# Optimization experiments

Measured on AMD Instinct MI355X. Metric: run time of the kernel, lower is better.

## Reference

```python
import math
import jax, jax.numpy as jnp
import numpy as np

ANCHORS_SETTINGS = (
    dict(layer='p3', stride=32, size=48, scale=[2 ** (1.0 / 3.0), 2 ** (2.0 / 3.0)], aspect_ratio=[0.667, 1, 1.5]),
    dict(layer='p4', stride=64, size=96, scale=[2 ** (1.0 / 3.0), 2 ** (2.0 / 3.0)], aspect_ratio=[0.667, 1, 1.5]),
    dict(layer='p5', stride=128, size=192, scale=[1, 2 ** (1.0 / 3.0), 2 ** (2.0 / 3.0)], aspect_ratio=[0.667, 1, 1.5]),
)


def anchor_configs():
    # 21 static (kernel, stride, padding) configs, in the exact counter order of
    # weighted_anchor_aggregator (p3 x6, p4 x6, p5 x9).
    cfgs = []
    for info in ANCHORS_SETTINGS:
        stride, size = info['stride'], info['size']
        for scale in info['scale']:
            for ar in info['aspect_ratio']:
                kernel = (int(size * scale / float(ar) ** 0.5), int(size * scale * float(ar) ** 0.5))
                padding = (math.ceil((kernel[0] - stride) / 2.0), math.ceil((kernel[1] - stride) / 2.0))
                cfgs.append((kernel, (stride, stride), padding))
    return cfgs


def extract_weighted_patches(x, weights, kernel, stride, padding):
    # x: (B,H,W,C); weights: (B,k,gh,gw). Vectorized equivalent of the original
    # lax.scan over per-position dynamic_slice gathers:
    #   acc = sum_{i,j} weights[:,:,i,j] (x) x_pad[:, i*s : i*s+kh, j*s : j*s+kw, :]
    b = x.shape[0]
    _, k, gh, gw = weights.shape
    xp = jnp.pad(x, ((0, 0),
                     (padding[0], padding[0] + kernel[0]),
                     (padding[1], padding[1] + kernel[1]),
                     (0, 0)))
    rows = jnp.arange(gh)[:, None] * stride[0] + jnp.arange(kernel[0])[None, :]  # (gh, kh)
    cols = jnp.arange(gw)[:, None] * stride[1] + jnp.arange(kernel[1])[None, :]  # (gw, kw)
    # gather all strided patches: (B, gh, kh, gw, kw, C)
    patches = xp[:, rows][:, :, :, cols]
    # weighted sum over grid positions -> (B, k, kh, kw, C)
    return jnp.einsum('bkij,bihjwc->bkhwc', weights, patches)


def _aggregate(x, weights_p3, weights_p4, weights_p5):
    weights = ([weights_p3[:, a] for a in range(weights_p3.shape[1])]
               + [weights_p4[:, a] for a in range(weights_p4.shape[1])]
               + [weights_p5[:, a] for a in range(weights_p5.shape[1])])
    b, k = weights[0].shape[0], weights[0].shape[1]
    acc = jnp.zeros((b * k, 224, 224, 3), x.dtype)
    for w, (kernel, stride, padding) in zip(weights, anchor_configs()):
        agg = extract_weighted_patches(x, w, kernel, stride, padding)
        agg = agg.reshape(b * k, kernel[0], kernel[1], 3)
        acc = acc + jax.image.resize(agg, (b * k, 224, 224, 3), 'bilinear')
    return acc


def setup_inputs() -> dict:
    key = jax.random.key(0)
    k0, k1, k2, k3 = jax.random.split(key, 4)
    B, K = 8, 4
    return {
        'x': jax.random.normal(k0, (B, 448, 448, 3), jnp.float32),
        'weights_p3': jax.random.uniform(k1, (B, 6, K, 14, 14), jnp.float32),
        'weights_p4': jax.random.uniform(k2, (B, 6, K, 7, 7), jnp.float32),
        'weights_p5': jax.random.uniform(k3, (B, 9, K, 4, 4), jnp.float32),
    }


def reference(x, weights_p3, weights_p4, weights_p5):
    return _aggregate(x, weights_p3, weights_p4, weights_p5)
```

## Files before the change

kernel.cpp:

```cpp
#include <hip/hip_runtime.h>
#include <math.h>


#define BATCH 8
#define KK 4
#define OUT_HW 224
#define IMG_HW 448
#define NCFG 21

#define WTBL_BYTES (NCFG * 2 * OUT_HW * 16)
#define ITBL_BYTES (NCFG * 2 * OUT_HW * 4)
#define WT_OFF_BYTES (WTBL_BYTES + ITBL_BYTES)
#define WT_F4 12912
#define AGG_OFF_BYTES (WT_OFF_BYTES + WT_F4 * 16)

struct CfgEntry {
    int kh, kw;
    int mth, mtw;
    int tbl;
    int ws_off;
};

struct GroupArgs {
    CfgEntry e[NCFG];
    int n;
};

struct ACfg {
    int kh, kw, p0, p1;
    int layer;
    int qpr;
    int wt_off;
    int ws_off;
    int block_start;
    int blocks_per_img;
};

struct AggArgs {
    ACfg e[NCFG];
    int n;
};

struct TablesArgs { int kh[NCFG]; int kw[NCFG]; };

struct TrArgs {
    int layer[NCFG];
    int anchor[NCFG];
    int gsz[NCFG];
    int wt_off[NCFG];
};

struct F3 { float a, b, c; };

__device__ inline unsigned int bf16_rne(float f) {
    unsigned int u = __float_as_uint(f);
    return (u + 0x7fffu + ((u >> 16) & 1u)) >> 16;
}

__global__ __launch_bounds__(256) void init_tables(float4* __restrict__ wtbl,
                                                   int* __restrict__ itbl,
                                                   TablesArgs t) {
    int cfg = blockIdx.x >> 1;
    int dim = blockIdx.x & 1;
    int o = threadIdx.x;
    if (o >= OUT_HW) return;
    int n = dim ? t.kw[cfg] : t.kh[cfg];

    float inv = (float)(1.0 / ((double)OUT_HW / (double)n));
    float ks  = inv > 1.f ? inv : 1.f;
    float rks = 1.f / ks;
    float sf  = ((float)o + 0.5f) * inv - 0.5f;
    int i0 = (int)ceilf(sf - ks);  if (i0 < 0) i0 = 0;
    int i1 = (int)floorf(sf + ks); if (i1 > n - 1) i1 = n - 1;
    float sum = 0.f;
    for (int i = i0; i <= i1; ++i) {
        float v = 1.f - fabsf((float)i - sf) * rks;
        sum += (v > 0.f ? v : 0.f);
    }
    float rsum = 1.f / sum;
    float w[4];
#pragma unroll
    for (int d = 0; d < 4; ++d) {
        int i = i0 + d;
        float v = 0.f;
        if (i <= i1) {
            v = 1.f - fabsf((float)i - sf) * rks;
            v = (v > 0.f ? v : 0.f) * rsum;
        }
        w[d] = v;
    }
    int idx = cfg * (2 * OUT_HW) + dim * OUT_HW + o;
    wtbl[idx] = make_float4(w[0], w[1], w[2], w[3]);
    itbl[idx] = i0;
}

__global__ __launch_bounds__(256) void transpose_w(
        const float* __restrict__ wp3, const float* __restrict__ wp4,
        const float* __restrict__ wp5, float4* __restrict__ wT, TrArgs t) {
    int cfg = blockIdx.x;
    int b = blockIdx.y;
    int gsz = t.gsz[cfg];
    const float* base;
    int A;
    if (t.layer[cfg] == 0)      { base = wp3; A = 6; }
    else if (t.layer[cfg] == 1) { base = wp4; A = 6; }
    else                        { base = wp5; A = 9; }
    const float* src = base + (size_t)(b * A + t.anchor[cfg]) * (KK * gsz);
    for (int g = threadIdx.x; g < gsz; g += 256) {
        wT[t.wt_off[cfg] + b * gsz + g] =
            make_float4(src[0 * gsz + g], src[1 * gsz + g],
                        src[2 * gsz + g], src[3 * gsz + g]);
    }
}

template <int GH, int GW, int STRIDE>
__device__ inline void agg_body(const ACfg& c, int b, int h, int w0,
                                const float* __restrict__ xb,
                                const float4* __restrict__ wlds,
                                uint2* __restrict__ agg) {
    float acc[2][4][3] = {};

    const int rb = h - c.p0;
    int ilo = rb >= 0 ? 0 : (-rb + STRIDE - 1) / STRIDE;
    int ihi = (IMG_HW - 1 - rb) / STRIDE;
    if (ihi > GH - 1) ihi = GH - 1;

    const int cb = w0 - c.p1;

#pragma unroll 1
    for (int i = ilo; i <= ihi; ++i) {
        const float* xr = xb + (size_t)(rb + i * STRIDE) * (IMG_HW * 3);
        const float4* wrow = wlds + i * GW;
#pragma unroll
        for (int j = 0; j < GW; ++j) {
            int col = cb + j * STRIDE;
            int cc0 = col;
            if (cc0 < 0) cc0 = 0;
            if (cc0 > IMG_HW - 1) cc0 = IMG_HW - 1;
            int cc1 = col + 1;
            if (cc1 < 0) cc1 = 0;
            if (cc1 > IMG_HW - 1) cc1 = IMG_HW - 1;
            F3 v0 = *(const F3*)(xr + (size_t)cc0 * 3);
            F3 v1 = *(const F3*)(xr + (size_t)cc1 * 3);
            bool k0 = (unsigned)col < (unsigned)IMG_HW;
            bool k1 = (unsigned)(col + 1) < (unsigned)IMG_HW;
            float x0 = k0 ? v0.a : 0.f;
            float x1 = k0 ? v0.b : 0.f;
            float x2 = k0 ? v0.c : 0.f;
            float y0 = k1 ? v1.a : 0.f;
            float y1 = k1 ? v1.b : 0.f;
            float y2 = k1 ? v1.c : 0.f;
            float4 wk = wrow[j];
            acc[0][0][0] = fmaf(wk.x, x0, acc[0][0][0]);
            acc[0][0][1] = fmaf(wk.x, x1, acc[0][0][1]);
            acc[0][0][2] = fmaf(wk.x, x2, acc[0][0][2]);
            acc[0][1][0] = fmaf(wk.y, x0, acc[0][1][0]);
            acc[0][1][1] = fmaf(wk.y, x1, acc[0][1][1]);
            acc[0][1][2] = fmaf(wk.y, x2, acc[0][1][2]);
            acc[0][2][0] = fmaf(wk.z, x0, acc[0][2][0]);
            acc[0][2][1] = fmaf(wk.z, x1, acc[0][2][1]);
            acc[0][2][2] = fmaf(wk.z, x2, acc[0][2][2]);
            acc[0][3][0] = fmaf(wk.w, x0, acc[0][3][0]);
            acc[0][3][1] = fmaf(wk.w, x1, acc[0][3][1]);
            acc[0][3][2] = fmaf(wk.w, x2, acc[0][3][2]);
            acc[1][0][0] = fmaf(wk.x, y0, acc[1][0][0]);
            acc[1][0][1] = fmaf(wk.x, y1, acc[1][0][1]);
            acc[1][0][2] = fmaf(wk.x, y2, acc[1][0][2]);
            acc[1][1][0] = fmaf(wk.y, y0, acc[1][1][0]);
            acc[1][1][1] = fmaf(wk.y, y1, acc[1][1][1]);
            acc[1][1][2] = fmaf(wk.y, y2, acc[1][1][2]);
            acc[1][2][0] = fmaf(wk.z, y0, acc[1][2][0]);
            acc[1][2][1] = fmaf(wk.z, y1, acc[1][2][1]);
            acc[1][2][2] = fmaf(wk.z, y2, acc[1][2][2]);
            acc[1][3][0] = fmaf(wk.w, y0, acc[1][3][0]);
            acc[1][3][1] = fmaf(wk.w, y1, acc[1][3][1]);
            acc[1][3][2] = fmaf(wk.w, y2, acc[1][3][2]);
        }
    }

    const int npix = c.kh * c.kw;
    const bool two = (w0 + 1) < c.kw;
#pragma unroll
    for (int k = 0; k < 4; ++k) {
        size_t base = (size_t)c.ws_off + (size_t)(b * KK + k) * npix
                    + (size_t)h * c.kw + w0;
        uint2 o0;
        o0.x = bf16_rne(acc[0][k][0]) | (bf16_rne(acc[0][k][1]) << 16);
        o0.y = bf16_rne(acc[0][k][2]);
        agg[base] = o0;
        if (two) {
            uint2 o1;
            o1.x = bf16_rne(acc[1][k][0]) | (bf16_rne(acc[1][k][1]) << 16);
            o1.y = bf16_rne(acc[1][k][2]);
            agg[base + 1] = o1;
        }
    }
}

__global__ __launch_bounds__(256, 4) void agg_all(
        const float* __restrict__ x,
        const float4* __restrict__ wT,
        uint2* __restrict__ agg,
        AggArgs a) {
    int bid = blockIdx.x;
    int ci = 0;
    while (ci + 1 < a.n && bid >= a.e[ci + 1].block_start) ci++;
    const ACfg c = a.e[ci];
    int local = bid - c.block_start;
    int b     = local / c.blocks_per_img;
    int sblk  = local - b * c.blocks_per_img;

    const int gsz = (c.layer == 0) ? 196 : (c.layer == 1) ? 49 : 16;
    __shared__ float4 wlds[196];
    for (int t = threadIdx.x; t < gsz; t += 256)
        wlds[t] = wT[c.wt_off + b * gsz + t];
    __syncthreads();

    int pidx = sblk * 256 + (int)threadIdx.x;
    if (pidx >= c.kh * c.qpr) return;
    int h  = pidx / c.qpr;
    int w0 = (pidx - h * c.qpr) * 2;

    const float* __restrict__ xb = x + (size_t)b * (IMG_HW * IMG_HW * 3);
    if (c.layer == 0)      agg_body<14, 14, 32>(c, b, h, w0, xb, wlds, agg);
    else if (c.layer == 1) agg_body<7, 7, 64>(c, b, h, w0, xb, wlds, agg);
    else                   agg_body<4, 4, 128>(c, b, h, w0, xb, wlds, agg);
}

template <int TH, int TW>
__device__ inline void taps_direct(const uint2* __restrict__ base,
                                   int kh, int kw, int i0, int j0,
                                   float4 wh4, float4 ww4,
                                   float& a0, float& a1, float& a2) {
    const float* wh = (const float*)&wh4;
    const float* ww = (const float*)&ww4;
    uint2 v[TH][TW];
#pragma unroll
    for (int d = 0; d < TH; ++d) {
        int gi = i0 + d;
        if (gi > kh - 1) gi = kh - 1;
        const uint2* rp = base + (size_t)gi * kw;
#pragma unroll
        for (int e = 0; e < TW; ++e) {
            int gj = j0 + e;
            if (gj > kw - 1) gj = kw - 1;
            v[d][e] = rp[gj];
        }
    }
#pragma unroll
    for (int d = 0; d < TH; ++d) {
        float r0 = 0.f, r1 = 0.f, r2 = 0.f;
#pragma unroll
        for (int e = 0; e < TW; ++e) {
            uint2 t = v[d][e];
            float c0 = __uint_as_float(t.x << 16);
            float c1 = __uint_as_float(t.x & 0xffff0000u);
            float c2 = __uint_as_float(t.y << 16);
            float w = ww[e];
            r0 = fmaf(w, c0, r0);
            r1 = fmaf(w, c1, r1);
            r2 = fmaf(w, c2, r2);
        }
        a0 = fmaf(wh[d], r0, a0);
        a1 = fmaf(wh[d], r1, a1);
        a2 = fmaf(wh[d], r2, a2);
    }
}

__global__ __launch_bounds__(256) void resize_kernel(
        const uint2* __restrict__ agg,
        const float4* __restrict__ wtbl,
        const int* __restrict__ itbl,
        float* __restrict__ out,
        GroupArgs g, int accumulate) {
    const int tid = threadIdx.x;
    const int tx = tid & 15;
    const int ty = tid >> 4;
    const int xo = blockIdx.x * 16 + tx;
    const int yo = blockIdx.y * 16 + ty;
    const int bk = blockIdx.z;

    __shared__ float4 wlds[NCFG * 32];
    __shared__ int    ilds[NCFG * 32];

    const int nent = g.n * 32;
    for (int e = tid; e < nent; e += 256) {
        int ci  = e >> 5;
        int r   = e & 31;
        int isW = r >> 4;
        int idx = r & 15;
        int base_o = isW ? (blockIdx.x * 16) : (blockIdx.y * 16);
        int src = g.e[ci].tbl * (2 * OUT_HW) + isW * OUT_HW + base_o + idx;
        wlds[ci * 32 + r] = wtbl[src];
        ilds[ci * 32 + r] = itbl[src];
    }
    __syncthreads();

    size_t ob = (((size_t)bk * OUT_HW + yo) * OUT_HW + xo) * 3;
    float a0, a1, a2;
    if (accumulate) {
        a0 = out[ob]; a1 = out[ob + 1]; a2 = out[ob + 2];
    } else {
        a0 = a1 = a2 = 0.f;
    }

    for (int c = 0; c < g.n; ++c) {
        const CfgEntry e = g.e[c];
        float4 wh4 = wlds[c * 32 + ty];
        float4 ww4 = wlds[c * 32 + 16 + tx];
        int i0 = ilds[c * 32 + ty];
        int j0 = ilds[c * 32 + 16 + tx];
        const uint2* base = agg + (size_t)e.ws_off
                          + (size_t)bk * ((size_t)e.kh * e.kw);

        switch ((e.mth << 2) | e.mtw) {
            case (2 << 2) | 2:
                taps_direct<2, 2>(base, e.kh, e.kw, i0, j0, wh4, ww4, a0, a1, a2);
                break;
            case (3 << 2) | 2:
                taps_direct<3, 2>(base, e.kh, e.kw, i0, j0, wh4, ww4, a0, a1, a2);
                break;
            case (2 << 2) | 3:
                taps_direct<2, 3>(base, e.kh, e.kw, i0, j0, wh4, ww4, a0, a1, a2);
                break;
            case (3 << 2) | 3:
                taps_direct<3, 3>(base, e.kh, e.kw, i0, j0, wh4, ww4, a0, a1, a2);
                break;
            case (4 << 2) | 3:
                taps_direct<4, 3>(base, e.kh, e.kw, i0, j0, wh4, ww4, a0, a1, a2);
                break;
            case (3 << 2) | 4:
                taps_direct<3, 4>(base, e.kh, e.kw, i0, j0, wh4, ww4, a0, a1, a2);
                break;
            default:
                taps_direct<4, 4>(base, e.kh, e.kw, i0, j0, wh4, ww4, a0, a1, a2);
                break;
        }
    }

    out[ob + 0] = a0; out[ob + 1] = a1; out[ob + 2] = a2;
}

extern "C" void kernel_launch(void* const* d_in, const int* in_sizes, int n_in,
                              void* d_out, int out_size, void* d_ws, size_t ws_size,
                              hipStream_t stream) {
    const float* x   = (const float*)d_in[0];
    const float* wp3 = (const float*)d_in[1];
    const float* wp4 = (const float*)d_in[2];
    const float* wp5 = (const float*)d_in[3];
    float* out = (float*)d_out;
    float4* wtbl = (float4*)d_ws;
    int*    itbl = (int*)((char*)d_ws + WTBL_BYTES);
    float4* wT   = (float4*)((char*)d_ws + WT_OFF_BYTES);
    uint2*  agg  = (uint2*)((char*)d_ws + AGG_OFF_BYTES);

    struct { int stride, size, nscale; double scales[3]; int gh; } layers[3] = {
        {32, 48, 2, {pow(2.0, 1.0 / 3.0), pow(2.0, 2.0 / 3.0), 0.0}, 14},
        {64, 96, 2, {pow(2.0, 1.0 / 3.0), pow(2.0, 2.0 / 3.0), 0.0}, 7},
        {128, 192, 3, {1.0, pow(2.0, 1.0 / 3.0), pow(2.0, 2.0 / 3.0)}, 4},
    };
    const double ars[3] = {0.667, 1.0, 1.5};

    struct HostCfg {
        int kh, kw, stride, p0, p1, gh, gw, layer, anchor, mth, mtw, wt_off;
        int qpr, blocks_per_img;
    } cfg[NCFG];
    TablesArgs ta;
    TrArgs tr;
    int nc = 0, wt_run = 0;
    for (int L = 0; L < 3; ++L) {
        int anchor = 0;
        for (int si = 0; si < layers[L].nscale; ++si) {
            for (int ai = 0; ai < 3; ++ai) {
                double ss = (double)layers[L].size * layers[L].scales[si];
                double sq = pow(ars[ai], 0.5);
                int kh = (int)(ss / sq);
                int kw = (int)(ss * sq);
                HostCfg& e = cfg[nc];
                e.kh = kh; e.kw = kw;
                e.stride = layers[L].stride;
                e.p0 = (int)ceil((double)(kh - layers[L].stride) / 2.0);
                e.p1 = (int)ceil((double)(kw - layers[L].stride) / 2.0);
                e.gh = layers[L].gh; e.gw = layers[L].gh;
                e.layer = L; e.anchor = anchor++;
                e.mth = (kh < OUT_HW) ? 2 : (int)((2.0 * kh) / OUT_HW) + 1;
                e.mtw = (kw < OUT_HW) ? 2 : (int)((2.0 * kw) / OUT_HW) + 1;
                if (e.mth > 4) e.mth = 4;
                if (e.mtw > 4) e.mtw = 4;
                e.qpr = (kw + 1) / 2;
                e.blocks_per_img = (kh * e.qpr + 255) / 256;
                e.wt_off = wt_run;
                int gsz = e.gh * e.gw;
                wt_run += BATCH * gsz;
                ta.kh[nc] = kh; ta.kw[nc] = kw;
                tr.layer[nc] = L; tr.anchor[nc] = e.anchor;
                tr.gsz[nc] = gsz; tr.wt_off[nc] = e.wt_off;
                ++nc;
            }
        }
    }

    init_tables<<<NCFG * 2, 256, 0, stream>>>(wtbl, itbl, ta);
    transpose_w<<<dim3(NCFG, BATCH), 256, 0, stream>>>(wp3, wp4, wp5, wT, tr);

    size_t cap_px = (ws_size - AGG_OFF_BYTES) / 8;
    dim3 rgrid(OUT_HW / 16, OUT_HW / 16, BATCH * KK);

    int i = 0;
    int first = 1;
    while (i < NCFG) {
        int gstart = i;
        size_t used = 0;
        while (i < NCFG) {
            size_t need = (size_t)cfg[i].kh * cfg[i].kw * (BATCH * KK);
            if (i > gstart && used + need > cap_px) break;
            used += need;
            ++i;
            if (used >= cap_px) break;
        }
        GroupArgs g; g.n = 0;
        AggArgs aa; aa.n = 0;
        int ablocks = 0;
        size_t off = 0;
        for (int c = gstart; c < i; ++c) {
            ACfg& lc = aa.e[aa.n++];
            lc.kh = cfg[c].kh; lc.kw = cfg[c].kw;
            lc.p0 = cfg[c].p0; lc.p1 = cfg[c].p1;
            lc.layer = cfg[c].layer;
            lc.qpr = cfg[c].qpr;
            lc.wt_off = cfg[c].wt_off;
            lc.ws_off = (int)off;
            lc.block_start = ablocks;
            lc.blocks_per_img = cfg[c].blocks_per_img;
            ablocks += cfg[c].blocks_per_img * BATCH;
            CfgEntry& re = g.e[g.n++];
            re.kh = cfg[c].kh; re.kw = cfg[c].kw;
            re.mth = cfg[c].mth; re.mtw = cfg[c].mtw;
            re.tbl = c; re.ws_off = (int)off;
            off += (size_t)cfg[c].kh * cfg[c].kw * (BATCH * KK);
        }
        agg_all<<<ablocks, 256, 0, stream>>>(x, wT, agg, aa);
        resize_kernel<<<rgrid, 256, 0, stream>>>(agg, wtbl, itbl, out, g, first ? 0 : 1);
        first = 0;
    }
    (void)in_sizes; (void)n_in; (void)out_size;
}
```

Measured before the change: 306.4 us.

## Resize 2x2 output pixels per thread with padded 16-byte tap loads

The resize kernel now has each thread compute a 2x2 output patch, so neighbouring outputs share loaded source taps. It reads the aggregate through 16-byte uint4 loads over a row layout padded to even width, and the aggregation kernel writes two pixels as one uint4 store. Blocks are remapped with an XCD-style interleave, batch and spatial block indices are swapped in agg_all, and weight/index tables are read directly from global memory instead of being staged in LDS. The costs are more registers, wider shifted-weight selection logic and slightly larger workspace rows.

```diff
diff --git a/kernel.cpp b/kernel.cpp
--- a/kernel.cpp
+++ b/kernel.cpp
@@ -14,8 +14,11 @@
 #define WT_F4 12912
 #define AGG_OFF_BYTES (WT_OFF_BYTES + WT_F4 * 16)
 
+#define RZ_BLOCKS (7 * 7 * BATCH * KK)
+#define RZ_CHUNK (RZ_BLOCKS / 8)
+
 struct CfgEntry {
-    int kh, kw;
+    int kh, kw, kwp;
     int mth, mtw;
     int tbl;
     int ws_off;
@@ -27,7 +30,7 @@
 };
 
 struct ACfg {
-    int kh, kw, p0, p1;
+    int kh, kw, kwp, p0, p1;
     int layer;
     int qpr;
     int wt_off;
@@ -178,22 +181,17 @@
         }
     }
 
-    const int npix = c.kh * c.kw;
-    const bool two = (w0 + 1) < c.kw;
+    const int npix = c.kh * c.kwp;
 #pragma unroll
     for (int k = 0; k < 4; ++k) {
         size_t base = (size_t)c.ws_off + (size_t)(b * KK + k) * npix
-                    + (size_t)h * c.kw + w0;
-        uint2 o0;
-        o0.x = bf16_rne(acc[0][k][0]) | (bf16_rne(acc[0][k][1]) << 16);
-        o0.y = bf16_rne(acc[0][k][2]);
-        agg[base] = o0;
-        if (two) {
-            uint2 o1;
-            o1.x = bf16_rne(acc[1][k][0]) | (bf16_rne(acc[1][k][1]) << 16);
-            o1.y = bf16_rne(acc[1][k][2]);
-            agg[base + 1] = o1;
-        }
+                    + (size_t)h * c.kwp + w0;
+        uint4 o;
+        o.x = bf16_rne(acc[0][k][0]) | (bf16_rne(acc[0][k][1]) << 16);
+        o.y = bf16_rne(acc[0][k][2]);
+        o.z = bf16_rne(acc[1][k][0]) | (bf16_rne(acc[1][k][1]) << 16);
+        o.w = bf16_rne(acc[1][k][2]);
+        *(uint4*)(agg + base) = o;
     }
 }
 
@@ -207,8 +205,8 @@
     while (ci + 1 < a.n && bid >= a.e[ci + 1].block_start) ci++;
     const ACfg c = a.e[ci];
     int local = bid - c.block_start;
-    int b     = local / c.blocks_per_img;
-    int sblk  = local - b * c.blocks_per_img;
+    int b     = local & 7;
+    int sblk  = local >> 3;
 
     const int gsz = (c.layer == 0) ? 196 : (c.layer == 1) ? 49 : 16;
     __shared__ float4 wlds[196];
@@ -227,43 +225,108 @@
     else                   agg_body<4, 4, 128>(c, b, h, w0, xb, wlds, agg);
 }
 
-template <int TH, int TW>
-__device__ inline void taps_direct(const uint2* __restrict__ base,
-                                   int kh, int kw, int i0, int j0,
-                                   float4 wh4, float4 ww4,
-                                   float& a0, float& a1, float& a2) {
-    const float* wh = (const float*)&wh4;
-    const float* ww = (const float*)&ww4;
-    uint2 v[TH][TW];
-#pragma unroll
-    for (int d = 0; d < TH; ++d) {
-        int gi = i0 + d;
-        if (gi > kh - 1) gi = kh - 1;
-        const uint2* rp = base + (size_t)gi * kw;
-#pragma unroll
-        for (int e = 0; e < TW; ++e) {
-            int gj = j0 + e;
-            if (gj > kw - 1) gj = kw - 1;
-            v[d][e] = rp[gj];
-        }
-    }
-#pragma unroll
-    for (int d = 0; d < TH; ++d) {
-        float r0 = 0.f, r1 = 0.f, r2 = 0.f;
-#pragma unroll
-        for (int e = 0; e < TW; ++e) {
-            uint2 t = v[d][e];
-            float c0 = __uint_as_float(t.x << 16);
-            float c1 = __uint_as_float(t.x & 0xffff0000u);
-            float c2 = __uint_as_float(t.y << 16);
-            float w = ww[e];
-            r0 = fmaf(w, c0, r0);
-            r1 = fmaf(w, c1, r1);
-            r2 = fmaf(w, c2, r2);
-        }
-        a0 = fmaf(wh[d], r0, a0);
-        a1 = fmaf(wh[d], r1, a1);
-        a2 = fmaf(wh[d], r2, a2);
+template <int NR, int NP>
+__device__ inline void taps4(const uint2* __restrict__ plane,
+                             int kh, int kwp,
+                             int i0a, int i0b, int j0a, int j0b,
+                             float4 wha, float4 whb,
+                             float4 wwa, float4 wwb,
+                             float (&acc)[2][2][3]) {
+    const int d0 = j0a & 1;
+    const int a0 = j0a - d0;
+    const int dj = j0b - a0;
+    const int di = i0b - i0a;
+
+    float wa[8], wb[8], ra[8], rb[8];
+#pragma unroll
+    for (int m = 0; m < 8; ++m) { wa[m] = 0.f; wb[m] = 0.f; ra[m] = 0.f; rb[m] = 0.f; }
+
+    {
+        bool s = d0 != 0;
+        wa[0] = s ? 0.f : wwa.x;
+        wa[1] = s ? wwa.x : wwa.y;
+        wa[2] = s ? wwa.y : wwa.z;
+        wa[3] = s ? wwa.z : wwa.w;
+        wa[4] = s ? wwa.w : 0.f;
+    }
+    {
+        bool s1 = (dj & 1) != 0, s2 = (dj & 2) != 0;
+        float t0 = s1 ? 0.f : wwb.x;
+        float t1 = s1 ? wwb.x : wwb.y;
+        float t2 = s1 ? wwb.y : wwb.z;
+        float t3 = s1 ? wwb.z : wwb.w;
+        float t4 = s1 ? wwb.w : 0.f;
+        wb[0] = s2 ? 0.f : t0;
+        wb[1] = s2 ? 0.f : t1;
+        wb[2] = s2 ? t0 : t2;
+        wb[3] = s2 ? t1 : t3;
+        wb[4] = s2 ? t2 : t4;
+        wb[5] = s2 ? t3 : 0.f;
+        wb[6] = s2 ? t4 : 0.f;
+    }
+    ra[0] = wha.x; ra[1] = wha.y; ra[2] = wha.z; ra[3] = wha.w;
+    {
+        bool s1 = (di & 1) != 0, s2 = (di & 2) != 0;
+        float t0 = s1 ? 0.f : whb.x;
+        float t1 = s1 ? whb.x : whb.y;
+        float t2 = s1 ? whb.y : whb.z;
+        float t3 = s1 ? whb.z : whb.w;
+        float t4 = s1 ? whb.w : 0.f;
+        rb[0] = s2 ? 0.f : t0;
+        rb[1] = s2 ? 0.f : t1;
+        rb[2] = s2 ? t0 : t2;
+        rb[3] = s2 ? t1 : t3;
+        rb[4] = s2 ? t2 : t4;
+        rb[5] = s2 ? t3 : 0.f;
+        rb[6] = s2 ? t4 : 0.f;
+    }
+
+    const int kh1 = kh - 1;
+    const int cmax = kwp - 2;
+#pragma unroll
+    for (int d = 0; d < NR; ++d) {
+        int r = i0a + d;
+        if (r > kh1) r = kh1;
+        const uint2* rowp = plane + (size_t)r * kwp;
+        uint4 v[NP];
+#pragma unroll
+        for (int p = 0; p < NP; ++p) {
+            int cc = a0 + 2 * p;
+            if (cc > cmax) cc = cmax;
+            v[p] = *(const uint4*)(rowp + cc);
+        }
+        float ca0 = 0.f, ca1 = 0.f, ca2 = 0.f;
+        float cb0 = 0.f, cb1 = 0.f, cb2 = 0.f;
+#pragma unroll
+        for (int p = 0; p < NP; ++p) {
+            float q00 = __uint_as_float(v[p].x << 16);
+            float q01 = __uint_as_float(v[p].x & 0xffff0000u);
+            float q02 = __uint_as_float(v[p].y << 16);
+            float q10 = __uint_as_float(v[p].z << 16);
+            float q11 = __uint_as_float(v[p].z & 0xffff0000u);
+            float q12 = __uint_as_float(v[p].w << 16);
+            float wA0 = wa[2 * p], wA1 = wa[2 * p + 1];
+            float wB0 = wb[2 * p], wB1 = wb[2 * p + 1];
+            ca0 = fmaf(wA0, q00, ca0); ca0 = fmaf(wA1, q10, ca0);
+            ca1 = fmaf(wA0, q01, ca1); ca1 = fmaf(wA1, q11, ca1);
+            ca2 = fmaf(wA0, q02, ca2); ca2 = fmaf(wA1, q12, ca2);
+            cb0 = fmaf(wB0, q00, cb0); cb0 = fmaf(wB1, q10, cb0);
+            cb1 = fmaf(wB0, q01, cb1); cb1 = fmaf(wB1, q11, cb1);
+            cb2 = fmaf(wB0, q02, cb2); cb2 = fmaf(wB1, q12, cb2);
+        }
+        float rA = ra[d], rB = rb[d];
+        acc[0][0][0] = fmaf(rA, ca0, acc[0][0][0]);
+        acc[0][0][1] = fmaf(rA, ca1, acc[0][0][1]);
+        acc[0][0][2] = fmaf(rA, ca2, acc[0][0][2]);
+        acc[0][1][0] = fmaf(rA, cb0, acc[0][1][0]);
+        acc[0][1][1] = fmaf(rA, cb1, acc[0][1][1]);
+        acc[0][1][2] = fmaf(rA, cb2, acc[0][1][2]);
+        acc[1][0][0] = fmaf(rB, ca0, acc[1][0][0]);
+        acc[1][0][1] = fmaf(rB, ca1, acc[1][0][1]);
+        acc[1][0][2] = fmaf(rB, ca2, acc[1][0][2]);
+        acc[1][1][0] = fmaf(rB, cb0, acc[1][1][0]);
+        acc[1][1][1] = fmaf(rB, cb1, acc[1][1][1]);
+        acc[1][1][2] = fmaf(rB, cb2, acc[1][1][2]);
     }
 }
 
@@ -273,72 +336,79 @@
         const int* __restrict__ itbl,
         float* __restrict__ out,
         GroupArgs g, int accumulate) {
+    int flat = blockIdx.x;
+    int wg = (flat & 7) * RZ_CHUNK + (flat >> 3);
+    int bx = wg % 7;
+    int tq = wg / 7;
+    int by = tq % 7;
+    int bk = tq / 7;
+
     const int tid = threadIdx.x;
     const int tx = tid & 15;
     const int ty = tid >> 4;
-    const int xo = blockIdx.x * 16 + tx;
-    const int yo = blockIdx.y * 16 + ty;
-    const int bk = blockIdx.z;
-
-    __shared__ float4 wlds[NCFG * 32];
-    __shared__ int    ilds[NCFG * 32];
-
-    const int nent = g.n * 32;
-    for (int e = tid; e < nent; e += 256) {
-        int ci  = e >> 5;
-        int r   = e & 31;
-        int isW = r >> 4;
-        int idx = r & 15;
-        int base_o = isW ? (blockIdx.x * 16) : (blockIdx.y * 16);
-        int src = g.e[ci].tbl * (2 * OUT_HW) + isW * OUT_HW + base_o + idx;
-        wlds[ci * 32 + r] = wtbl[src];
-        ilds[ci * 32 + r] = itbl[src];
-    }
-    __syncthreads();
-
-    size_t ob = (((size_t)bk * OUT_HW + yo) * OUT_HW + xo) * 3;
-    float a0, a1, a2;
+    const int xo = bx * 32 + tx * 2;
+    const int yo = by * 32 + ty * 2;
+
+    float acc[2][2][3] = {};
+    size_t ob0 = (((size_t)bk * OUT_HW + yo) * OUT_HW + xo) * 3;
+    size_t ob1 = ob0 + OUT_HW * 3;
     if (accumulate) {
-        a0 = out[ob]; a1 = out[ob + 1]; a2 = out[ob + 2];
-    } else {
-        a0 = a1 = a2 = 0.f;
+#pragma unroll
+        for (int ch = 0; ch < 3; ++ch) {
+            acc[0][0][ch] = out[ob0 + ch];
+            acc[0][1][ch] = out[ob0 + 3 + ch];
+            acc[1][0][ch] = out[ob1 + ch];
+            acc[1][1][ch] = out[ob1 + 3 + ch];
+        }
     }
 
     for (int c = 0; c < g.n; ++c) {
         const CfgEntry e = g.e[c];
-        float4 wh4 = wlds[c * 32 + ty];
-        float4 ww4 = wlds[c * 32 + 16 + tx];
-        int i0 = ilds[c * 32 + ty];
-        int j0 = ilds[c * 32 + 16 + tx];
-        const uint2* base = agg + (size_t)e.ws_off
-                          + (size_t)bk * ((size_t)e.kh * e.kw);
+        const float4* wrow = wtbl + e.tbl * (2 * OUT_HW);
+        const int*    irow = itbl + e.tbl * (2 * OUT_HW);
+        float4 wha = wrow[yo];
+        float4 whb = wrow[yo + 1];
+        float4 wwa = wrow[OUT_HW + xo];
+        float4 wwb = wrow[OUT_HW + xo + 1];
+        int i0a = irow[yo];
+        int i0b = irow[yo + 1];
+        int j0a = irow[OUT_HW + xo];
+        int j0b = irow[OUT_HW + xo + 1];
+        const uint2* plane = agg + (size_t)e.ws_off
+                           + (size_t)bk * ((size_t)e.kh * e.kwp);
 
         switch ((e.mth << 2) | e.mtw) {
             case (2 << 2) | 2:
-                taps_direct<2, 2>(base, e.kh, e.kw, i0, j0, wh4, ww4, a0, a1, a2);
-                break;
+                taps4<3, 2>(plane, e.kh, e.kwp, i0a, i0b, j0a, j0b,
+                            wha, whb, wwa, wwb, acc); break;
             case (3 << 2) | 2:
-                taps_direct<3, 2>(base, e.kh, e.kw, i0, j0, wh4, ww4, a0, a1, a2);
-                break;
+                taps4<5, 2>(plane, e.kh, e.kwp, i0a, i0b, j0a, j0b,
+                            wha, whb, wwa, wwb, acc); break;
             case (2 << 2) | 3:
-                taps_direct<2, 3>(base, e.kh, e.kw, i0, j0, wh4, ww4, a0, a1, a2);
-                break;
+                taps4<3, 3>(plane, e.kh, e.kwp, i0a, i0b, j0a, j0b,
+                            wha, whb, wwa, wwb, acc); break;
             case (3 << 2) | 3:
-                taps_direct<3, 3>(base, e.kh, e.kw, i0, j0, wh4, ww4, a0, a1, a2);
-                break;
+                taps4<5, 3>(plane, e.kh, e.kwp, i0a, i0b, j0a, j0b,
+                            wha, whb, wwa, wwb, acc); break;
             case (4 << 2) | 3:
-                taps_direct<4, 3>(base, e.kh, e.kw, i0, j0, wh4, ww4, a0, a1, a2);
-                break;
+                taps4<6, 3>(plane, e.kh, e.kwp, i0a, i0b, j0a, j0b,
+                            wha, whb, wwa, wwb, acc); break;
             case (3 << 2) | 4:
-                taps_direct<3, 4>(base, e.kh, e.kw, i0, j0, wh4, ww4, a0, a1, a2);
-                break;
+                taps4<5, 4>(plane, e.kh, e.kwp, i0a, i0b, j0a, j0b,
+                            wha, whb, wwa, wwb, acc); break;
             default:
-                taps_direct<4, 4>(base, e.kh, e.kw, i0, j0, wh4, ww4, a0, a1, a2);
-                break;
-        }
-    }
-
-    out[ob + 0] = a0; out[ob + 1] = a1; out[ob + 2] = a2;
+                taps4<6, 4>(plane, e.kh, e.kwp, i0a, i0b, j0a, j0b,
+                            wha, whb, wwa, wwb, acc); break;
+        }
+    }
+
+#pragma unroll
+    for (int ch = 0; ch < 3; ++ch) {
+        out[ob0 + ch]     = acc[0][0][ch];
+        out[ob0 + 3 + ch] = acc[0][1][ch];
+        out[ob1 + ch]     = acc[1][0][ch];
+        out[ob1 + 3 + ch] = acc[1][1][ch];
+    }
 }
 
 extern "C" void kernel_launch(void* const* d_in, const int* in_sizes, int n_in,
@@ -362,7 +432,7 @@
     const double ars[3] = {0.667, 1.0, 1.5};
 
     struct HostCfg {
-        int kh, kw, stride, p0, p1, gh, gw, layer, anchor, mth, mtw, wt_off;
+        int kh, kw, kwp, stride, p0, p1, gh, gw, layer, anchor, mth, mtw, wt_off;
         int qpr, blocks_per_img;
     } cfg[NCFG];
     TablesArgs ta;
@@ -378,6 +448,7 @@
                 int kw = (int)(ss * sq);
                 HostCfg& e = cfg[nc];
                 e.kh = kh; e.kw = kw;
+                e.kwp = kw + (kw & 1);
                 e.stride = layers[L].stride;
                 e.p0 = (int)ceil((double)(kh - layers[L].stride) / 2.0);
                 e.p1 = (int)ceil((double)(kw - layers[L].stride) / 2.0);
@@ -387,7 +458,7 @@
                 e.mtw = (kw < OUT_HW) ? 2 : (int)((2.0 * kw) / OUT_HW) + 1;
                 if (e.mth > 4) e.mth = 4;
                 if (e.mtw > 4) e.mtw = 4;
-                e.qpr = (kw + 1) / 2;
+                e.qpr = e.kwp / 2;
                 e.blocks_per_img = (kh * e.qpr + 255) / 256;
                 e.wt_off = wt_run;
                 int gsz = e.gh * e.gw;
@@ -404,7 +475,7 @@
     transpose_w<<<dim3(NCFG, BATCH), 256, 0, stream>>>(wp3, wp4, wp5, wT, tr);
 
     size_t cap_px = (ws_size - AGG_OFF_BYTES) / 8;
-    dim3 rgrid(OUT_HW / 16, OUT_HW / 16, BATCH * KK);
+    dim3 rgrid(RZ_BLOCKS);
 
     int i = 0;
     int first = 1;
@@ -412,7 +483,7 @@
         int gstart = i;
         size_t used = 0;
         while (i < NCFG) {
-            size_t need = (size_t)cfg[i].kh * cfg[i].kw * (BATCH * KK);
+            size_t need = (size_t)cfg[i].kh * cfg[i].kwp * (BATCH * KK);
             if (i > gstart && used + need > cap_px) break;
             used += need;
             ++i;
@@ -424,7 +495,7 @@
         size_t off = 0;
         for (int c = gstart; c < i; ++c) {
             ACfg& lc = aa.e[aa.n++];
-            lc.kh = cfg[c].kh; lc.kw = cfg[c].kw;
+            lc.kh = cfg[c].kh; lc.kw = cfg[c].kw; lc.kwp = cfg[c].kwp;
             lc.p0 = cfg[c].p0; lc.p1 = cfg[c].p1;
             lc.layer = cfg[c].layer;
             lc.qpr = cfg[c].qpr;
@@ -434,10 +505,10 @@
             lc.blocks_per_img = cfg[c].blocks_per_img;
             ablocks += cfg[c].blocks_per_img * BATCH;
             CfgEntry& re = g.e[g.n++];
-            re.kh = cfg[c].kh; re.kw = cfg[c].kw;
+            re.kh = cfg[c].kh; re.kw = cfg[c].kw; re.kwp = cfg[c].kwp;
             re.mth = cfg[c].mth; re.mtw = cfg[c].mtw;
             re.tbl = c; re.ws_off = (int)off;
-            off += (size_t)cfg[c].kh * cfg[c].kw * (BATCH * KK);
+            off += (size_t)cfg[c].kh * cfg[c].kwp * (BATCH * KK);
         }
         agg_all<<<ablocks, 256, 0, stream>>>(x, wT, agg, aa);
         resize_kernel<<<rgrid, 256, 0, stream>>>(agg, wtbl, itbl, out, g, first ? 0 : 1);
```

New measurement: 335.8 us. 1.1x slower.

## Pad aggregate rows to even width, use packed FMA and 16-byte stores

Applied to the files above, without the earlier changes.

Pads each aggregate row to an even width so every thread writes its two adjacent pixels as one aligned 16-byte store, with no tail branch. The accumulation is rewritten with two-wide float vectors so the compiler can emit packed FMA instructions. It also reorders the agg block index so the batch comes from the low bits, replacing a division, and caps the per-group workspace size, which may change how configs are split into groups. The padding adds a little workspace traffic, and the resize kernel now indexes rows by the padded width.

```diff
diff --git a/kernel.cpp b/kernel.cpp
--- a/kernel.cpp
+++ b/kernel.cpp
@@ -14,8 +14,12 @@
 #define WT_F4 12912
 #define AGG_OFF_BYTES (WT_OFF_BYTES + WT_F4 * 16)
 
+#define GROUP_PX_CAP 9200000
+
+typedef float v2f __attribute__((ext_vector_type(2)));
+
 struct CfgEntry {
-    int kh, kw;
+    int kh, kw, kwp;
     int mth, mtw;
     int tbl;
     int ws_off;
@@ -27,7 +31,7 @@
 };
 
 struct ACfg {
-    int kh, kw, p0, p1;
+    int kh, kw, kwp, p0, p1;
     int layer;
     int qpr;
     int wt_off;
@@ -118,7 +122,11 @@
                                 const float* __restrict__ xb,
                                 const float4* __restrict__ wlds,
                                 uint2* __restrict__ agg) {
-    float acc[2][4][3] = {};
+    v2f acc2[4][3];
+#pragma unroll
+    for (int k = 0; k < 4; ++k)
+#pragma unroll
+        for (int ch = 0; ch < 3; ++ch) { acc2[k][ch].x = 0.f; acc2[k][ch].y = 0.f; }
 
     const int rb = h - c.p0;
     int ilo = rb >= 0 ? 0 : (-rb + STRIDE - 1) / STRIDE;
@@ -134,66 +142,49 @@
 #pragma unroll
         for (int j = 0; j < GW; ++j) {
             int col = cb + j * STRIDE;
-            int cc0 = col;
-            if (cc0 < 0) cc0 = 0;
-            if (cc0 > IMG_HW - 1) cc0 = IMG_HW - 1;
-            int cc1 = col + 1;
-            if (cc1 < 0) cc1 = 0;
-            if (cc1 > IMG_HW - 1) cc1 = IMG_HW - 1;
+            unsigned cc0 = (unsigned)col;
+            if (cc0 > (unsigned)(IMG_HW - 1)) cc0 = (unsigned)(IMG_HW - 1);
+            unsigned cc1 = (unsigned)(col + 1);
+            if (cc1 > (unsigned)(IMG_HW - 1)) cc1 = (unsigned)(IMG_HW - 1);
             F3 v0 = *(const F3*)(xr + (size_t)cc0 * 3);
             F3 v1 = *(const F3*)(xr + (size_t)cc1 * 3);
             bool k0 = (unsigned)col < (unsigned)IMG_HW;
             bool k1 = (unsigned)(col + 1) < (unsigned)IMG_HW;
-            float x0 = k0 ? v0.a : 0.f;
-            float x1 = k0 ? v0.b : 0.f;
-            float x2 = k0 ? v0.c : 0.f;
-            float y0 = k1 ? v1.a : 0.f;
-            float y1 = k1 ? v1.b : 0.f;
-            float y2 = k1 ? v1.c : 0.f;
+            v2f d0, d1, d2;
+            d0.x = k0 ? v0.a : 0.f;  d0.y = k1 ? v1.a : 0.f;
+            d1.x = k0 ? v0.b : 0.f;  d1.y = k1 ? v1.b : 0.f;
+            d2.x = k0 ? v0.c : 0.f;  d2.y = k1 ? v1.c : 0.f;
             float4 wk = wrow[j];
-            acc[0][0][0] = fmaf(wk.x, x0, acc[0][0][0]);
-            acc[0][0][1] = fmaf(wk.x, x1, acc[0][0][1]);
-            acc[0][0][2] = fmaf(wk.x, x2, acc[0][0][2]);
-            acc[0][1][0] = fmaf(wk.y, x0, acc[0][1][0]);
-            acc[0][1][1] = fmaf(wk.y, x1, acc[0][1][1]);
-            acc[0][1][2] = fmaf(wk.y, x2, acc[0][1][2]);
-            acc[0][2][0] = fmaf(wk.z, x0, acc[0][2][0]);
-            acc[0][2][1] = fmaf(wk.z, x1, acc[0][2][1]);
-            acc[0][2][2] = fmaf(wk.z, x2, acc[0][2][2]);
-            acc[0][3][0] = fmaf(wk.w, x0, acc[0][3][0]);
-            acc[0][3][1] = fmaf(wk.w, x1, acc[0][3][1]);
-            acc[0][3][2] = fmaf(wk.w, x2, acc[0][3][2]);
-            acc[1][0][0] = fmaf(wk.x, y0, acc[1][0][0]);
-            acc[1][0][1] = fmaf(wk.x, y1, acc[1][0][1]);
-            acc[1][0][2] = fmaf(wk.x, y2, acc[1][0][2]);
-            acc[1][1][0] = fmaf(wk.y, y0, acc[1][1][0]);
-            acc[1][1][1] = fmaf(wk.y, y1, acc[1][1][1]);
-            acc[1][1][2] = fmaf(wk.y, y2, acc[1][1][2]);
-            acc[1][2][0] = fmaf(wk.z, y0, acc[1][2][0]);
-            acc[1][2][1] = fmaf(wk.z, y1, acc[1][2][1]);
-            acc[1][2][2] = fmaf(wk.z, y2, acc[1][2][2]);
-            acc[1][3][0] = fmaf(wk.w, y0, acc[1][3][0]);
-            acc[1][3][1] = fmaf(wk.w, y1, acc[1][3][1]);
-            acc[1][3][2] = fmaf(wk.w, y2, acc[1][3][2]);
-        }
-    }
-
-    const int npix = c.kh * c.kw;
-    const bool two = (w0 + 1) < c.kw;
+            v2f wv0 = {wk.x, wk.x};
+            v2f wv1 = {wk.y, wk.y};
+            v2f wv2 = {wk.z, wk.z};
+            v2f wv3 = {wk.w, wk.w};
+            acc2[0][0] = __builtin_elementwise_fma(wv0, d0, acc2[0][0]);
+            acc2[0][1] = __builtin_elementwise_fma(wv0, d1, acc2[0][1]);
+            acc2[0][2] = __builtin_elementwise_fma(wv0, d2, acc2[0][2]);
+            acc2[1][0] = __builtin_elementwise_fma(wv1, d0, acc2[1][0]);
+            acc2[1][1] = __builtin_elementwise_fma(wv1, d1, acc2[1][1]);
+            acc2[1][2] = __builtin_elementwise_fma(wv1, d2, acc2[1][2]);
+            acc2[2][0] = __builtin_elementwise_fma(wv2, d0, acc2[2][0]);
+            acc2[2][1] = __builtin_elementwise_fma(wv2, d1, acc2[2][1]);
+            acc2[2][2] = __builtin_elementwise_fma(wv2, d2, acc2[2][2]);
+            acc2[3][0] = __builtin_elementwise_fma(wv3, d0, acc2[3][0]);
+            acc2[3][1] = __builtin_elementwise_fma(wv3, d1, acc2[3][1]);
+            acc2[3][2] = __builtin_elementwise_fma(wv3, d2, acc2[3][2]);
+        }
+    }
+
+    const int npix = c.kh * c.kwp;
 #pragma unroll
     for (int k = 0; k < 4; ++k) {
         size_t base = (size_t)c.ws_off + (size_t)(b * KK + k) * npix
-                    + (size_t)h * c.kw + w0;
-        uint2 o0;
-        o0.x = bf16_rne(acc[0][k][0]) | (bf16_rne(acc[0][k][1]) << 16);
-        o0.y = bf16_rne(acc[0][k][2]);
-        agg[base] = o0;
-        if (two) {
-            uint2 o1;
-            o1.x = bf16_rne(acc[1][k][0]) | (bf16_rne(acc[1][k][1]) << 16);
-            o1.y = bf16_rne(acc[1][k][2]);
-            agg[base + 1] = o1;
-        }
+                    + (size_t)h * c.kwp + w0;
+        uint4 o;
+        o.x = bf16_rne(acc2[k][0].x) | (bf16_rne(acc2[k][1].x) << 16);
+        o.y = bf16_rne(acc2[k][2].x);
+        o.z = bf16_rne(acc2[k][0].y) | (bf16_rne(acc2[k][1].y) << 16);
+        o.w = bf16_rne(acc2[k][2].y);
+        *(uint4*)(agg + base) = o;
     }
 }
 
@@ -207,8 +198,8 @@
     while (ci + 1 < a.n && bid >= a.e[ci + 1].block_start) ci++;
     const ACfg c = a.e[ci];
     int local = bid - c.block_start;
-    int b     = local / c.blocks_per_img;
-    int sblk  = local - b * c.blocks_per_img;
+    int b     = local & 7;
+    int sblk  = local >> 3;
 
     const int gsz = (c.layer == 0) ? 196 : (c.layer == 1) ? 49 : 16;
     __shared__ float4 wlds[196];
@@ -229,7 +220,7 @@
 
 template <int TH, int TW>
 __device__ inline void taps_direct(const uint2* __restrict__ base,
-                                   int kh, int kw, int i0, int j0,
+                                   int kh, int kw, int kwp, int i0, int j0,
                                    float4 wh4, float4 ww4,
                                    float& a0, float& a1, float& a2) {
     const float* wh = (const float*)&wh4;
@@ -239,7 +230,7 @@
     for (int d = 0; d < TH; ++d) {
         int gi = i0 + d;
         if (gi > kh - 1) gi = kh - 1;
-        const uint2* rp = base + (size_t)gi * kw;
+        const uint2* rp = base + (size_t)gi * kwp;
 #pragma unroll
         for (int e = 0; e < TW; ++e) {
             int gj = j0 + e;
@@ -311,29 +302,29 @@
         int i0 = ilds[c * 32 + ty];
         int j0 = ilds[c * 32 + 16 + tx];
         const uint2* base = agg + (size_t)e.ws_off
-                          + (size_t)bk * ((size_t)e.kh * e.kw);
+                          + (size_t)bk * ((size_t)e.kh * e.kwp);
 
         switch ((e.mth << 2) | e.mtw) {
             case (2 << 2) | 2:
-                taps_direct<2, 2>(base, e.kh, e.kw, i0, j0, wh4, ww4, a0, a1, a2);
+                taps_direct<2, 2>(base, e.kh, e.kw, e.kwp, i0, j0, wh4, ww4, a0, a1, a2);
                 break;
             case (3 << 2) | 2:
-                taps_direct<3, 2>(base, e.kh, e.kw, i0, j0, wh4, ww4, a0, a1, a2);
+                taps_direct<3, 2>(base, e.kh, e.kw, e.kwp, i0, j0, wh4, ww4, a0, a1, a2);
                 break;
             case (2 << 2) | 3:
-                taps_direct<2, 3>(base, e.kh, e.kw, i0, j0, wh4, ww4, a0, a1, a2);
+                taps_direct<2, 3>(base, e.kh, e.kw, e.kwp, i0, j0, wh4, ww4, a0, a1, a2);
                 break;
             case (3 << 2) | 3:
-                taps_direct<3, 3>(base, e.kh, e.kw, i0, j0, wh4, ww4, a0, a1, a2);
+                taps_direct<3, 3>(base, e.kh, e.kw, e.kwp, i0, j0, wh4, ww4, a0, a1, a2);
                 break;
             case (4 << 2) | 3:
-                taps_direct<4, 3>(base, e.kh, e.kw, i0, j0, wh4, ww4, a0, a1, a2);
+                taps_direct<4, 3>(base, e.kh, e.kw, e.kwp, i0, j0, wh4, ww4, a0, a1, a2);
                 break;
             case (3 << 2) | 4:
-                taps_direct<3, 4>(base, e.kh, e.kw, i0, j0, wh4, ww4, a0, a1, a2);
+                taps_direct<3, 4>(base, e.kh, e.kw, e.kwp, i0, j0, wh4, ww4, a0, a1, a2);
                 break;
             default:
-                taps_direct<4, 4>(base, e.kh, e.kw, i0, j0, wh4, ww4, a0, a1, a2);
+                taps_direct<4, 4>(base, e.kh, e.kw, e.kwp, i0, j0, wh4, ww4, a0, a1, a2);
                 break;
         }
     }
@@ -362,7 +353,7 @@
     const double ars[3] = {0.667, 1.0, 1.5};
 
     struct HostCfg {
-        int kh, kw, stride, p0, p1, gh, gw, layer, anchor, mth, mtw, wt_off;
+        int kh, kw, kwp, stride, p0, p1, gh, gw, layer, anchor, mth, mtw, wt_off;
         int qpr, blocks_per_img;
     } cfg[NCFG];
     TablesArgs ta;
@@ -378,6 +369,7 @@
                 int kw = (int)(ss * sq);
                 HostCfg& e = cfg[nc];
                 e.kh = kh; e.kw = kw;
+                e.kwp = kw + (kw & 1);
                 e.stride = layers[L].stride;
                 e.p0 = (int)ceil((double)(kh - layers[L].stride) / 2.0);
                 e.p1 = (int)ceil((double)(kw - layers[L].stride) / 2.0);
@@ -387,7 +379,7 @@
                 e.mtw = (kw < OUT_HW) ? 2 : (int)((2.0 * kw) / OUT_HW) + 1;
                 if (e.mth > 4) e.mth = 4;
                 if (e.mtw > 4) e.mtw = 4;
-                e.qpr = (kw + 1) / 2;
+                e.qpr = e.kwp / 2;
                 e.blocks_per_img = (kh * e.qpr + 255) / 256;
                 e.wt_off = wt_run;
                 int gsz = e.gh * e.gw;
@@ -404,6 +396,7 @@
     transpose_w<<<dim3(NCFG, BATCH), 256, 0, stream>>>(wp3, wp4, wp5, wT, tr);
 
     size_t cap_px = (ws_size - AGG_OFF_BYTES) / 8;
+    if (cap_px > (size_t)GROUP_PX_CAP) cap_px = (size_t)GROUP_PX_CAP;
     dim3 rgrid(OUT_HW / 16, OUT_HW / 16, BATCH * KK);
 
     int i = 0;
@@ -412,7 +405,7 @@
         int gstart = i;
         size_t used = 0;
         while (i < NCFG) {
-            size_t need = (size_t)cfg[i].kh * cfg[i].kw * (BATCH * KK);
+            size_t need = (size_t)cfg[i].kh * cfg[i].kwp * (BATCH * KK);
             if (i > gstart && used + need > cap_px) break;
             used += need;
             ++i;
@@ -424,7 +417,7 @@
         size_t off = 0;
         for (int c = gstart; c < i; ++c) {
             ACfg& lc = aa.e[aa.n++];
-            lc.kh = cfg[c].kh; lc.kw = cfg[c].kw;
+            lc.kh = cfg[c].kh; lc.kw = cfg[c].kw; lc.kwp = cfg[c].kwp;
             lc.p0 = cfg[c].p0; lc.p1 = cfg[c].p1;
             lc.layer = cfg[c].layer;
             lc.qpr = cfg[c].qpr;
@@ -434,10 +427,10 @@
             lc.blocks_per_img = cfg[c].blocks_per_img;
             ablocks += cfg[c].blocks_per_img * BATCH;
             CfgEntry& re = g.e[g.n++];
-            re.kh = cfg[c].kh; re.kw = cfg[c].kw;
+            re.kh = cfg[c].kh; re.kw = cfg[c].kw; re.kwp = cfg[c].kwp;
             re.mth = cfg[c].mth; re.mtw = cfg[c].mtw;
             re.tbl = c; re.ws_off = (int)off;
-            off += (size_t)cfg[c].kh * cfg[c].kw * (BATCH * KK);
+            off += (size_t)cfg[c].kh * cfg[c].kwp * (BATCH * KK);
         }
         agg_all<<<ablocks, 256, 0, stream>>>(x, wT, agg, aa);
         resize_kernel<<<rgrid, 256, 0, stream>>>(agg, wtbl, itbl, out, g, first ? 0 : 1);
```

New measurement: 280.7 us. 8.4% less time.
